# Optimization experiments

Measured on AMD Instinct MI355X. Metric: run time of the kernel, lower is better.

The kernel has to match this reference:

```python
import jax, jax.numpy as jnp
import numpy as np

WINDOW = 5
PAD = WINDOW // 2


def _extract_patches(x):
    # x: (B,C,H,W) -> patches (B,C,K*K,H,W) with reflect padding, matching
    # F.pad(mode='reflect') + F.unfold(window, padding=0).
    B, C, H, W = x.shape
    xp = jnp.pad(x, ((0, 0), (0, 0), (PAD, PAD), (PAD, PAD)), mode='reflect')
    patches = jnp.stack(
        [xp[:, :, i:i + H, j:j + W] for i in range(WINDOW) for j in range(WINDOW)],
        axis=2,
    )
    return patches


def setup_inputs() -> dict:
    key = jax.random.key(0)
    k1, k2, k3 = jax.random.split(key, 3)
    x = jax.random.normal(k1, (4, 32, 256, 256), dtype=jnp.float32)
    mix = jax.random.normal(k2, (1, 32, 1, 1), dtype=jnp.float32)
    beta_raw = jax.random.normal(k3, (), dtype=jnp.float32)
    return {"x": x, "mix": mix, "beta_raw": beta_raw}


def reference(x, mix, beta_raw):
    patches = _extract_patches(x)  # (B,C,25,H,W)

    # Max filter (= max_pool2d over reflect-padded input, stride 1)
    max_out = jnp.max(patches, axis=2)

    # Soft (differentiable) median filter
    beta = 5.0 + 45.0 * jax.nn.sigmoid(beta_raw)
    center = jnp.mean(patches, axis=2, keepdims=True)
    weights = jax.nn.softmax(-beta * jnp.abs(patches - center), axis=2)
    median_out = jnp.sum(weights * patches, axis=2)

    lambda_c = jax.nn.sigmoid(mix)  # (1,C,1,1)
    return lambda_c * median_out + (1.0 - lambda_c) * max_out
```

## Files before the change

kernel.cpp:

```cpp
#include <hip/hip_runtime.h>
#include <math.h>

#define HW 256
#define TW 64
#define TH 32
#define LW 68
#define LH 36

__device__ __forceinline__ int reflect_idx(int i) {
    i = (i < 0) ? -i : i;
    i = (i >= HW) ? (2 * HW - 2 - i) : i;
    return i;
}

__device__ __forceinline__ float4 max4(float4 a, float4 b) {
    float4 r; r.x = fmaxf(a.x, b.x); r.y = fmaxf(a.y, b.y);
    r.z = fmaxf(a.z, b.z); r.w = fmaxf(a.w, b.w); return r;
}
__device__ __forceinline__ float4 max34(float4 a, float4 b, float4 c) {
    float4 r; r.x = fmaxf(fmaxf(a.x, b.x), c.x); r.y = fmaxf(fmaxf(a.y, b.y), c.y);
    r.z = fmaxf(fmaxf(a.z, b.z), c.z); r.w = fmaxf(fmaxf(a.w, b.w), c.w); return r;
}
__device__ __forceinline__ float4 add4(float4 a, float4 b) {
    float4 r; r.x = a.x + b.x; r.y = a.y + b.y;
    r.z = a.z + b.z; r.w = a.w + b.w; return r;
}
__device__ __forceinline__ float4 sub4(float4 a, float4 b) {
    float4 r; r.x = a.x - b.x; r.y = a.y - b.y;
    r.z = a.z - b.z; r.w = a.w - b.w; return r;
}

__device__ __forceinline__ void proc_row(
    float4 A0, float4 B0, float4 A1, float4 B1, float4 A2, float4 B2,
    float4 A3, float4 B3, float4 A4, float4 B4,
    float4 cmA, float4 cmB, float4 csA, float4 csB,
    float bp, float c04b, float inv_bp, float lam,
    float* __restrict__ orow)
{
    const float cs[8] = {csA.x,csA.y,csA.z,csA.w, csB.x,csB.y,csB.z,csB.w};
    const float cm[8] = {cmA.x,cmA.y,cmA.z,cmA.w, cmB.x,cmB.y,cmB.z,cmB.w};
    const float vv[5][8] = {
        {A0.x,A0.y,A0.z,A0.w, B0.x,B0.y,B0.z,B0.w},
        {A1.x,A1.y,A1.z,A1.w, B1.x,B1.y,B1.z,B1.w},
        {A2.x,A2.y,A2.z,A2.w, B2.x,B2.y,B2.z,B2.w},
        {A3.x,A3.y,A3.z,A3.w, B3.x,B3.y,B3.z,B3.w},
        {A4.x,A4.y,A4.z,A4.w, B4.x,B4.y,B4.z,B4.w}};

    const float t12 = cs[1] + cs[2];
    const float t34 = cs[3] + cs[4];
    const float t56 = cs[5] + cs[6];
    const float u   = t12 + t34;
    const float w_  = t34 + t56;
    const float S[4] = {cs[0] + u, u + cs[5], cs[2] + w_, w_ + cs[7]};

    const float h12 = fmaxf(cm[1], cm[2]);
    const float h34 = fmaxf(cm[3], cm[4]);
    const float h56 = fmaxf(cm[5], cm[6]);
    const float m[4] = {fmaxf(fmaxf(cm[0], h12), h34),
                        fmaxf(fmaxf(h12, h34), cm[5]),
                        fmaxf(fmaxf(cm[2], h34), h56),
                        fmaxf(fmaxf(h34, h56), cm[7])};

    float bm[4], ws[4], wa[4];
    #pragma unroll
    for (int p = 0; p < 4; ++p) { bm[p] = S[p] * c04b; ws[p] = 0.0f; wa[p] = 0.0f; }

    #pragma unroll
    for (int k = 0; k < 5; ++k) {
        #pragma unroll
        for (int j = 0; j < 5; ++j) {
            #pragma unroll
            for (int p = 0; p < 4; ++p) {
                const float tv = fmaf(bp, vv[k][p + j], -bm[p]);
                const float e  = __builtin_amdgcn_exp2f(-fabsf(tv));
                ws[p] += e;
                wa[p] = fmaf(e, tv, wa[p]);
            }
        }
    }

    float4 o4;
    float o[4];
    #pragma unroll
    for (int p = 0; p < 4; ++p) {
        const float mean = S[p] * 0.04f;
        const float med  = fmaf(wa[p] * __builtin_amdgcn_rcpf(ws[p]), inv_bp, mean);
        o[p] = fmaf(lam, med - m[p], m[p]);
    }
    o4.x = o[0]; o4.y = o[1]; o4.z = o[2]; o4.w = o[3];
    *(float4*)orow = o4;
}

__global__ __launch_bounds__(256, 4)
void maxmedian_kernel(const float* __restrict__ x,
                      const float* __restrict__ mix,
                      const float* __restrict__ beta_raw,
                      float* __restrict__ out,
                      int C) {
    __shared__ __align__(16) float tile[LH * LW];

    const int tiles_x = HW / TW;
    const int tiles_per_plane = tiles_x * (HW / TH);
    const int plane = blockIdx.x / tiles_per_plane;
    const int t     = blockIdx.x % tiles_per_plane;
    const int ty0 = (t / tiles_x) * TH;
    const int tx0 = (t % tiles_x) * TW;

    const float* __restrict__ xp = x + (size_t)plane * (HW * HW);
    const int tid = threadIdx.x;

    {
        const int c   = tid & 63;
        const int r0s = tid >> 6;
        const int gx  = tx0 + c;
        #pragma unroll
        for (int k = 0; k < 9; ++k) {
            const int r  = r0s + 4 * k;
            const int gy = reflect_idx(ty0 + r - 2);
            tile[r * LW + c + 2] = xp[gy * HW + gx];
        }
        if (tid < 144) {
            const int jj = tid & 3;
            const int j  = (jj < 2) ? jj : (64 + jj);
            const int r  = tid >> 2;
            const int gx2 = reflect_idx(tx0 + j - 2);
            const int gy2 = reflect_idx(ty0 + r - 2);
            tile[r * LW + j] = xp[gy2 * HW + gx2];
        }
    }
    __syncthreads();

    const int ch = plane % C;
    const float lam  = 1.0f / (1.0f + __expf(-mix[ch]));
    const float beta = 5.0f + 45.0f / (1.0f + __expf(-beta_raw[0]));
    const float bp     = beta * 1.44269504088896f;
    const float inv_bp = 1.0f / bp;
    const float c04b   = 0.04f * bp;

    const int tx  = tid & 15;
    const int ryq = tid >> 4;
    const int r0  = ryq * 2;
    const float* lbase = &tile[r0 * LW + 4 * tx];

    float4 w0a = *(const float4*)(lbase + 0 * LW);
    float4 w0b = *(const float4*)(lbase + 0 * LW + 4);
    float4 w1a = *(const float4*)(lbase + 1 * LW);
    float4 w1b = *(const float4*)(lbase + 1 * LW + 4);
    float4 w2a = *(const float4*)(lbase + 2 * LW);
    float4 w2b = *(const float4*)(lbase + 2 * LW + 4);
    float4 w3a = *(const float4*)(lbase + 3 * LW);
    float4 w3b = *(const float4*)(lbase + 3 * LW + 4);
    float4 w4a = *(const float4*)(lbase + 4 * LW);
    float4 w4b = *(const float4*)(lbase + 4 * LW + 4);
    float4 w5a = *(const float4*)(lbase + 5 * LW);
    float4 w5b = *(const float4*)(lbase + 5 * LW + 4);

    float4 csA = add4(add4(add4(w0a, w1a), add4(w2a, w3a)), w4a);
    float4 csB = add4(add4(add4(w0b, w1b), add4(w2b, w3b)), w4b);

    const float4 p12a = max4(w1a, w2a), p12b = max4(w1b, w2b);
    const float4 p34a = max4(w3a, w4a), p34b = max4(w3b, w4b);
    const float4 cm0a = max34(w0a, p12a, p34a);
    const float4 cm0b = max34(w0b, p12b, p34b);

    float* __restrict__ orow =
        out + (size_t)plane * (HW * HW) + (size_t)(ty0 + r0) * HW + (tx0 + 4 * tx);

    proc_row(w0a,w0b, w1a,w1b, w2a,w2b, w3a,w3b, w4a,w4b,
             cm0a, cm0b, csA, csB, bp, c04b, inv_bp, lam, orow);

    csA = add4(csA, sub4(w5a, w0a));
    csB = add4(csB, sub4(w5b, w0b));
    const float4 cm1a = max34(p12a, p34a, w5a);
    const float4 cm1b = max34(p12b, p34b, w5b);

    proc_row(w1a,w1b, w2a,w2b, w3a,w3b, w4a,w4b, w5a,w5b,
             cm1a, cm1b, csA, csB, bp, c04b, inv_bp, lam, orow + HW);
}

extern "C" void kernel_launch(void* const* d_in, const int* in_sizes, int n_in,
                              void* d_out, int out_size, void* d_ws, size_t ws_size,
                              hipStream_t stream) {
    const float* x        = (const float*)d_in[0];
    const float* mix      = (const float*)d_in[1];
    const float* beta_raw = (const float*)d_in[2];
    float* out            = (float*)d_out;

    const int planes = in_sizes[0] / (HW * HW);
    const int C      = in_sizes[1];
    const int tiles_per_plane = (HW / TW) * (HW / TH);
    const int grid = planes * tiles_per_plane;

    maxmedian_kernel<<<grid, 256, 0, stream>>>(x, mix, beta_raw, out, C);
}
```

Before: 39.57 us.

## Make blocks persistent over four row tiles with double-buffered register-staged LDS prefetch

Each block now processes four vertically stacked 32x64 tiles instead of one, which cuts the grid from 4096 blocks to 1024. The global loads for the next tile are issued into registers before computing the current tile, then written to the alternate LDS buffer, so load latency overlaps with the exp-heavy compute. The cost is more LDS and register pressure, fewer blocks to hide latency across CUs, and a serial dependency chain within each block.

Result: slower. 57.46 us (+45.2%).

```diff
diff --git a/kernel.cpp b/kernel.cpp
--- a/kernel.cpp
+++ b/kernel.cpp
@@ -6,6 +6,7 @@
 #define TH 32
 #define LW 68
 #define LH 36
+#define NT 4
 
 __device__ __forceinline__ int reflect_idx(int i) {
     i = (i < 0) ? -i : i;
@@ -79,7 +80,6 @@
         }
     }
 
-    float4 o4;
     float o[4];
     #pragma unroll
     for (int p = 0; p < 4; ++p) {
@@ -87,8 +87,44 @@
         const float med  = fmaf(wa[p] * __builtin_amdgcn_rcpf(ws[p]), inv_bp, mean);
         o[p] = fmaf(lam, med - m[p], m[p]);
     }
-    o4.x = o[0]; o4.y = o[1]; o4.z = o[2]; o4.w = o[3];
+    float4 o4; o4.x = o[0]; o4.y = o[1]; o4.z = o[2]; o4.w = o[3];
     *(float4*)orow = o4;
+}
+
+__device__ __forceinline__ void stage_regs(
+    const float* __restrict__ xp, int ty0, int tx0, int tid,
+    float pm[9], float& ph)
+{
+    const int c   = tid & 63;
+    const int r0s = tid >> 6;
+    const int gx  = tx0 + c;
+    #pragma unroll
+    for (int k = 0; k < 9; ++k) {
+        const int r  = r0s + 4 * k;
+        const int gy = reflect_idx(ty0 + r - 2);
+        pm[k] = xp[gy * HW + gx];
+    }
+    if (tid < 144) {
+        const int jj = tid & 3;
+        const int j  = (jj < 2) ? jj : (64 + jj);
+        const int r  = tid >> 2;
+        ph = xp[reflect_idx(ty0 + r - 2) * HW + reflect_idx(tx0 + j - 2)];
+    }
+}
+
+__device__ __forceinline__ void write_lds(
+    float* __restrict__ buf, int tid, const float pm[9], float ph)
+{
+    const int c   = tid & 63;
+    const int r0s = tid >> 6;
+    #pragma unroll
+    for (int k = 0; k < 9; ++k)
+        buf[(r0s + 4 * k) * LW + c + 2] = pm[k];
+    if (tid < 144) {
+        const int jj = tid & 3;
+        const int j  = (jj < 2) ? jj : (64 + jj);
+        buf[(tid >> 2) * LW + j] = ph;
+    }
 }
 
 __global__ __launch_bounds__(256, 4)
@@ -97,38 +133,15 @@
                       const float* __restrict__ beta_raw,
                       float* __restrict__ out,
                       int C) {
-    __shared__ __align__(16) float tile[LH * LW];
-
-    const int tiles_x = HW / TW;
-    const int tiles_per_plane = tiles_x * (HW / TH);
-    const int plane = blockIdx.x / tiles_per_plane;
-    const int t     = blockIdx.x % tiles_per_plane;
-    const int ty0 = (t / tiles_x) * TH;
-    const int tx0 = (t % tiles_x) * TW;
+    __shared__ __align__(16) float buf[2][LH * LW];
+
+    const int plane   = blockIdx.x >> 3;
+    const int rem     = blockIdx.x & 7;
+    const int tx0     = (rem >> 1) * TW;
+    const int ty_base = (rem & 1) * (NT * TH);
 
     const float* __restrict__ xp = x + (size_t)plane * (HW * HW);
     const int tid = threadIdx.x;
-
-    {
-        const int c   = tid & 63;
-        const int r0s = tid >> 6;
-        const int gx  = tx0 + c;
-        #pragma unroll
-        for (int k = 0; k < 9; ++k) {
-            const int r  = r0s + 4 * k;
-            const int gy = reflect_idx(ty0 + r - 2);
-            tile[r * LW + c + 2] = xp[gy * HW + gx];
-        }
-        if (tid < 144) {
-            const int jj = tid & 3;
-            const int j  = (jj < 2) ? jj : (64 + jj);
-            const int r  = tid >> 2;
-            const int gx2 = reflect_idx(tx0 + j - 2);
-            const int gy2 = reflect_idx(ty0 + r - 2);
-            tile[r * LW + j] = xp[gy2 * HW + gx2];
-        }
-    }
-    __syncthreads();
 
     const int ch = plane % C;
     const float lam  = 1.0f / (1.0f + __expf(-mix[ch]));
@@ -140,42 +153,63 @@
     const int tx  = tid & 15;
     const int ryq = tid >> 4;
     const int r0  = ryq * 2;
-    const float* lbase = &tile[r0 * LW + 4 * tx];
-
-    float4 w0a = *(const float4*)(lbase + 0 * LW);
-    float4 w0b = *(const float4*)(lbase + 0 * LW + 4);
-    float4 w1a = *(const float4*)(lbase + 1 * LW);
-    float4 w1b = *(const float4*)(lbase + 1 * LW + 4);
-    float4 w2a = *(const float4*)(lbase + 2 * LW);
-    float4 w2b = *(const float4*)(lbase + 2 * LW + 4);
-    float4 w3a = *(const float4*)(lbase + 3 * LW);
-    float4 w3b = *(const float4*)(lbase + 3 * LW + 4);
-    float4 w4a = *(const float4*)(lbase + 4 * LW);
-    float4 w4b = *(const float4*)(lbase + 4 * LW + 4);
-    float4 w5a = *(const float4*)(lbase + 5 * LW);
-    float4 w5b = *(const float4*)(lbase + 5 * LW + 4);
-
-    float4 csA = add4(add4(add4(w0a, w1a), add4(w2a, w3a)), w4a);
-    float4 csB = add4(add4(add4(w0b, w1b), add4(w2b, w3b)), w4b);
-
-    const float4 p12a = max4(w1a, w2a), p12b = max4(w1b, w2b);
-    const float4 p34a = max4(w3a, w4a), p34b = max4(w3b, w4b);
-    const float4 cm0a = max34(w0a, p12a, p34a);
-    const float4 cm0b = max34(w0b, p12b, p34b);
-
-    float* __restrict__ orow =
-        out + (size_t)plane * (HW * HW) + (size_t)(ty0 + r0) * HW + (tx0 + 4 * tx);
-
-    proc_row(w0a,w0b, w1a,w1b, w2a,w2b, w3a,w3b, w4a,w4b,
-             cm0a, cm0b, csA, csB, bp, c04b, inv_bp, lam, orow);
-
-    csA = add4(csA, sub4(w5a, w0a));
-    csB = add4(csB, sub4(w5b, w0b));
-    const float4 cm1a = max34(p12a, p34a, w5a);
-    const float4 cm1b = max34(p12b, p34b, w5b);
-
-    proc_row(w1a,w1b, w2a,w2b, w3a,w3b, w4a,w4b, w5a,w5b,
-             cm1a, cm1b, csA, csB, bp, c04b, inv_bp, lam, orow + HW);
+
+    float pm[9];
+    float ph = 0.0f;
+
+    stage_regs(xp, ty_base, tx0, tid, pm, ph);
+    write_lds(buf[0], tid, pm, ph);
+    __syncthreads();
+
+    #pragma unroll 1
+    for (int t = 0; t < NT; ++t) {
+        const int ty0 = ty_base + t * TH;
+
+        if (t < NT - 1)
+            stage_regs(xp, ty0 + TH, tx0, tid, pm, ph);
+
+        const float* lbase = &buf[t & 1][r0 * LW + 4 * tx];
+
+        float4 w0a = *(const float4*)(lbase + 0 * LW);
+        float4 w0b = *(const float4*)(lbase + 0 * LW + 4);
+        float4 w1a = *(const float4*)(lbase + 1 * LW);
+        float4 w1b = *(const float4*)(lbase + 1 * LW + 4);
+        float4 w2a = *(const float4*)(lbase + 2 * LW);
+        float4 w2b = *(const float4*)(lbase + 2 * LW + 4);
+        float4 w3a = *(const float4*)(lbase + 3 * LW);
+        float4 w3b = *(const float4*)(lbase + 3 * LW + 4);
+        float4 w4a = *(const float4*)(lbase + 4 * LW);
+        float4 w4b = *(const float4*)(lbase + 4 * LW + 4);
+        float4 w5a = *(const float4*)(lbase + 5 * LW);
+        float4 w5b = *(const float4*)(lbase + 5 * LW + 4);
+
+        float4 csA = add4(add4(add4(w0a, w1a), add4(w2a, w3a)), w4a);
+        float4 csB = add4(add4(add4(w0b, w1b), add4(w2b, w3b)), w4b);
+
+        const float4 p12a = max4(w1a, w2a), p12b = max4(w1b, w2b);
+        const float4 p34a = max4(w3a, w4a), p34b = max4(w3b, w4b);
+        const float4 cm0a = max34(w0a, p12a, p34a);
+        const float4 cm0b = max34(w0b, p12b, p34b);
+
+        float* __restrict__ orow =
+            out + (size_t)plane * (HW * HW) + (size_t)(ty0 + r0) * HW + (tx0 + 4 * tx);
+
+        proc_row(w0a,w0b, w1a,w1b, w2a,w2b, w3a,w3b, w4a,w4b,
+                 cm0a, cm0b, csA, csB, bp, c04b, inv_bp, lam, orow);
+
+        csA = add4(csA, sub4(w5a, w0a));
+        csB = add4(csB, sub4(w5b, w0b));
+        const float4 cm1a = max34(p12a, p34a, w5a);
+        const float4 cm1b = max34(p12b, p34b, w5b);
+
+        proc_row(w1a,w1b, w2a,w2b, w3a,w3b, w4a,w4b, w5a,w5b,
+                 cm1a, cm1b, csA, csB, bp, c04b, inv_bp, lam, orow + HW);
+
+        if (t < NT - 1) {
+            write_lds(buf[(t + 1) & 1], tid, pm, ph);
+            __syncthreads();
+        }
+    }
 }
 
 extern "C" void kernel_launch(void* const* d_in, const int* in_sizes, int n_in,
@@ -188,8 +222,7 @@
 
     const int planes = in_sizes[0] / (HW * HW);
     const int C      = in_sizes[1];
-    const int tiles_per_plane = (HW / TW) * (HW / TH);
-    const int grid = planes * tiles_per_plane;
+    const int grid = planes * 8;
 
     maxmedian_kernel<<<grid, 256, 0, stream>>>(x, mix, beta_raw, out, C);
 }
```

## Give each wavefront its own private halo tile to drop block barrier

Applied to the files above, without the earlier changes.

The shared tile is split into four per-wavefront tiles of 12 rows each. Each wave loads its own 8 output rows plus the 4-row halo and syncs with a wave barrier instead of __syncthreads. This removes cross-wave synchronization so waves can start computing independently. In exchange, halo rows are loaded redundantly (48 vs 36 rows per block) and LDS use rises.

New measurement: 40.25 us. Within noise of the previous version (+1.7%).

```diff
diff --git a/kernel.cpp b/kernel.cpp
--- a/kernel.cpp
+++ b/kernel.cpp
@@ -5,7 +5,7 @@
 #define TW 64
 #define TH 32
 #define LW 68
-#define LH 36
+#define WLH 12
 
 __device__ __forceinline__ int reflect_idx(int i) {
     i = (i < 0) ? -i : i;
@@ -79,7 +79,6 @@
         }
     }
 
-    float4 o4;
     float o[4];
     #pragma unroll
     for (int p = 0; p < 4; ++p) {
@@ -87,7 +86,7 @@
         const float med  = fmaf(wa[p] * __builtin_amdgcn_rcpf(ws[p]), inv_bp, mean);
         o[p] = fmaf(lam, med - m[p], m[p]);
     }
-    o4.x = o[0]; o4.y = o[1]; o4.z = o[2]; o4.w = o[3];
+    float4 o4; o4.x = o[0]; o4.y = o[1]; o4.z = o[2]; o4.w = o[3];
     *(float4*)orow = o4;
 }
 
@@ -97,7 +96,7 @@
                       const float* __restrict__ beta_raw,
                       float* __restrict__ out,
                       int C) {
-    __shared__ __align__(16) float tile[LH * LW];
+    __shared__ __align__(16) float wtile[4][WLH * LW];
 
     const int tiles_x = HW / TW;
     const int tiles_per_plane = tiles_x * (HW / TH);
@@ -107,28 +106,30 @@
     const int tx0 = (t % tiles_x) * TW;
 
     const float* __restrict__ xp = x + (size_t)plane * (HW * HW);
-    const int tid = threadIdx.x;
+    const int tid  = threadIdx.x;
+    const int wave = tid >> 6;
+    const int lane = tid & 63;
+
+    const int wy0 = ty0 + 8 * wave;
+    float* __restrict__ wt = wtile[wave];
 
     {
-        const int c   = tid & 63;
-        const int r0s = tid >> 6;
-        const int gx  = tx0 + c;
+        const int gx = tx0 + lane;
         #pragma unroll
-        for (int k = 0; k < 9; ++k) {
-            const int r  = r0s + 4 * k;
-            const int gy = reflect_idx(ty0 + r - 2);
-            tile[r * LW + c + 2] = xp[gy * HW + gx];
+        for (int k = 0; k < WLH; ++k) {
+            const int gy = reflect_idx(wy0 - 2 + k);
+            wt[k * LW + lane + 2] = xp[gy * HW + gx];
         }
-        if (tid < 144) {
-            const int jj = tid & 3;
+        if (lane < 48) {
+            const int jj = lane & 3;
             const int j  = (jj < 2) ? jj : (64 + jj);
-            const int r  = tid >> 2;
+            const int r  = lane >> 2;
             const int gx2 = reflect_idx(tx0 + j - 2);
-            const int gy2 = reflect_idx(ty0 + r - 2);
-            tile[r * LW + j] = xp[gy2 * HW + gx2];
+            const int gy2 = reflect_idx(wy0 - 2 + r);
+            wt[r * LW + j] = xp[gy2 * HW + gx2];
         }
     }
-    __syncthreads();
+    __builtin_amdgcn_wave_barrier();
 
     const int ch = plane % C;
     const float lam  = 1.0f / (1.0f + __expf(-mix[ch]));
@@ -137,10 +138,10 @@
     const float inv_bp = 1.0f / bp;
     const float c04b   = 0.04f * bp;
 
-    const int tx  = tid & 15;
-    const int ryq = tid >> 4;
+    const int tx  = lane & 15;
+    const int ryq = lane >> 4;
     const int r0  = ryq * 2;
-    const float* lbase = &tile[r0 * LW + 4 * tx];
+    const float* lbase = &wt[r0 * LW + 4 * tx];
 
     float4 w0a = *(const float4*)(lbase + 0 * LW);
     float4 w0b = *(const float4*)(lbase + 0 * LW + 4);
@@ -164,7 +165,7 @@
     const float4 cm0b = max34(w0b, p12b, p34b);
 
     float* __restrict__ orow =
-        out + (size_t)plane * (HW * HW) + (size_t)(ty0 + r0) * HW + (tx0 + 4 * tx);
+        out + (size_t)plane * (HW * HW) + (size_t)(wy0 + r0) * HW + (tx0 + 4 * tx);
 
     proc_row(w0a,w0b, w1a,w1b, w2a,w2b, w3a,w3b, w4a,w4b,
              cm0a, cm0b, csA, csB, bp, c04b, inv_bp, lam, orow);
```
